# Performance work log

Hardware: AMD Instinct MI355X
Metric: run time of the kernel (lower is better)

The kernel has to match this reference:

```python
import jax, jax.numpy as jnp
import numpy as np

B, L, D = 2048, 128, 100  # utterances, max words, input_dim
H = D // 2                # LSTM hidden per direction
K = 3                     # causes per emotion in label3


def setup_inputs() -> dict:
    key = jax.random.key(0)
    ks = jax.random.split(key, 16)
    s = 1.0 / np.sqrt(H)
    inp = {
        "word_encode": jax.random.normal(ks[0], (B, L, D), jnp.float32),
        "sen_lengths": jax.random.randint(ks[1], (B, 1), 1, L + 1),
        # deterministic alternating masks -> static n_emo = n_cau = B//2
        "bi_label_emo": (jnp.arange(B) % 2 == 0).astype(jnp.int32),
        "bi_label_cau": (jnp.arange(B) % 2 == 1).astype(jnp.int32),
        "label3": jax.random.randint(ks[2], (B // 2, 1, K), 0, B // 2),
        "W_ih_f": jax.random.uniform(ks[3], (4 * H, D), jnp.float32, -s, s),
        "W_hh_f": jax.random.uniform(ks[4], (4 * H, H), jnp.float32, -s, s),
        "b_ih_f": jax.random.uniform(ks[5], (4 * H,), jnp.float32, -s, s),
        "b_hh_f": jax.random.uniform(ks[6], (4 * H,), jnp.float32, -s, s),
        "W_ih_b": jax.random.uniform(ks[7], (4 * H, D), jnp.float32, -s, s),
        "W_hh_b": jax.random.uniform(ks[8], (4 * H, H), jnp.float32, -s, s),
        "b_ih_b": jax.random.uniform(ks[9], (4 * H,), jnp.float32, -s, s),
        "b_hh_b": jax.random.uniform(ks[10], (4 * H,), jnp.float32, -s, s),
        "W3_w": jax.random.normal(ks[11], (D, 3 * D + 1), jnp.float32) * 0.05,
        "W3_b": jnp.zeros((D,), jnp.float32),
        "cls_w": jax.random.normal(ks[12], (2, D), jnp.float32) * 0.05,
        "cls_b": jnp.zeros((2,), jnp.float32),
    }
    return inp


def _lstm_cell(x, h, c, W_ih, W_hh, b_ih, b_hh):
    # PyTorch gate order: i, f, g, o
    g = x @ W_ih.T + b_ih + h @ W_hh.T + b_hh
    i, f, gg, o = jnp.split(g, 4, axis=-1)
    c_new = jax.nn.sigmoid(f) * c + jax.nn.sigmoid(i) * jnp.tanh(gg)
    h_new = jax.nn.sigmoid(o) * jnp.tanh(c_new)
    return h_new, c_new


def reference(word_encode, sen_lengths, bi_label_emo, bi_label_cau, label3,
              W_ih_f, W_hh_f, b_ih_f, b_hh_f,
              W_ih_b, W_hh_b, b_ih_b, b_hh_b,
              W3_w, W3_b, cls_w, cls_b):
    lengths = sen_lengths.reshape(-1)  # [B]
    x = word_encode.astype(jnp.float32)

    # Forward-direction LSTM over packed sequence: carry freezes past each
    # sequence's length, so the final carry h equals h at t = len-1.
    xs = jnp.swapaxes(x, 0, 1)                         # [L, B, D]
    tmask = (jnp.arange(L)[:, None] < lengths[None, :])  # [L, B]

    def step(carry, inp):
        h, c = carry
        x_t, m = inp
        h_new, c_new = _lstm_cell(x_t, h, c, W_ih_f, W_hh_f, b_ih_f, b_hh_f)
        m = m[:, None]
        return (jnp.where(m, h_new, h), jnp.where(m, c_new, c)), None

    h0 = jnp.zeros((x.shape[0], H), jnp.float32)
    (h_fwd, _), _ = jax.lax.scan(step, (h0, h0), (xs, tmask))

    # Backward direction of a packed bi-LSTM: at t = len-1 the backward cell
    # has processed exactly one token (x[len-1]) starting from zero state.
    x_last = x[jnp.arange(x.shape[0]), lengths - 1]    # [B, D]
    h_bwd, _ = _lstm_cell(x_last, h0, h0, W_ih_b, W_hh_b, b_ih_b, b_hh_b)

    U = jnp.concatenate([h_fwd, h_bwd], axis=-1)       # [B, D]

    # masks are static constants -> host-side index extraction
    emo_idx = np.flatnonzero(np.asarray(bi_label_emo))
    cau_idx = np.flatnonzero(np.asarray(bi_label_cau))
    E = U[emo_idx]                                     # [ne, D]
    C = U[cau_idx]                                     # [nc, D]
    ne, nc = E.shape[0], C.shape[0]

    # fused pairwise item_att: cat(x, y, ||x-y||_2, x*y) -> [ne, nc, 3D+1]
    Eb = jnp.broadcast_to(E[:, None, :], (ne, nc, D))
    Cb = jnp.broadcast_to(C[None, :, :], (ne, nc, D))
    diff = E[:, None, :] - C[None, :, :]
    item2 = jnp.sqrt(jnp.sum(diff * diff, axis=-1, keepdims=True))
    pair = jnp.concatenate([Eb, Cb, item2, Eb * Cb], axis=-1)
    pair = pair.reshape(ne * nc, 3 * D + 1)

    h = jax.nn.sigmoid(pair @ W3_w.T + W3_b)           # dropout = identity (eval)
    logits = h @ cls_w.T + cls_b
    p = jax.nn.log_softmax(logits, axis=1).reshape(-1, 2)

    # label_pair[j*nc + i] = 1 if i in label3[j]
    lbl = label3.reshape(ne, -1)                       # [ne, K]
    label_pair = (lbl[:, :, None] == jnp.arange(nc)[None, None, :]).any(axis=1)
    label_pair = label_pair.astype(jnp.float32).reshape(-1)
    return (p, label_pair)
```

## Files before the change

kernel.cpp:

```cpp
#include <hip/hip_runtime.h>
#include <hip/hip_bf16.h>
#include <math.h>

#define B_  2048
#define L_  128
#define D_  100
#define H_  50
#define NE  1024
#define NC  1024
#define NP  (NE*NC)
#define GSTR 212

typedef __attribute__((ext_vector_type(8))) _Float16 half8v;
typedef __attribute__((ext_vector_type(4))) _Float16 half4v;
typedef __attribute__((ext_vector_type(4))) float f32x4;

__device__ __forceinline__ float sigf(float x) { return 1.f / (1.f + __expf(-x)); }
__device__ __forceinline__ float tanhfast(float x) {
  float e = __expf(-2.f * x);
  return (1.f - e) / (1.f + e);
}
__device__ __forceinline__ void bar_sync() {
  asm volatile("s_waitcnt lgkmcnt(0)" ::: "memory");
  __builtin_amdgcn_s_barrier();
  __builtin_amdgcn_sched_barrier(0);
}

__global__ __launch_bounds__(256) void k_build_idx(const int* __restrict__ emo,
                                                   const int* __restrict__ cau,
                                                   int* __restrict__ emo_idx,
                                                   int* __restrict__ cau_idx) {
  __shared__ int pe[256], pc[256];
  int tid = threadIdx.x;
  int ce = 0, cc = 0;
  int base = tid * 8;
  for (int r = 0; r < 8; r++) { ce += (emo[base + r] != 0); cc += (cau[base + r] != 0); }
  pe[tid] = ce; pc[tid] = cc;
  __syncthreads();
  if (tid == 0) {
    int re = 0, rc = 0;
    for (int i = 0; i < 256; i++) {
      int t = pe[i]; pe[i] = re; re += t;
      t = pc[i]; pc[i] = rc; rc += t;
    }
  }
  __syncthreads();
  int oe = pe[tid], oc = pc[tid];
  for (int r = 0; r < 8; r++) {
    int idx = base + r;
    if (emo[idx] != 0) emo_idx[oe++] = idx;
    if (cau[idx] != 0) cau_idx[oc++] = idx;
  }
}

__global__ __launch_bounds__(256) void k_lstm_fwd(const float* __restrict__ x,
                                                  const int* __restrict__ lens,
                                                  const float* __restrict__ Wih,
                                                  const float* __restrict__ Whh,
                                                  const float* __restrict__ bih,
                                                  const float* __restrict__ bhh,
                                                  float* __restrict__ U) {
  __shared__ __align__(16) _Float16 Wihf[13 * 4 * 64 * 8];
  __shared__ __align__(16) _Float16 Whhf[13 * 2 * 64 * 8];
  __shared__ __align__(16) _Float16 xs[2][16 * 128];
  __shared__ __align__(16) _Float16 hs[16 * 64];
  __shared__ float gbuf[8 * GSTR];
  __shared__ float bias_l[200];
  __shared__ int len_l[8];
  int tid = threadIdx.x;
  int b0 = blockIdx.x * 8;

  for (int id = tid; id < 13 * 4 * 64; id += 256) {
    int l = id & 63, ks = (id >> 6) & 3, n = id >> 8;
    int j = n * 16 + (l & 15);
    int kb = ks * 32 + (l >> 4) * 8;
    half8v v;
    #pragma unroll
    for (int e = 0; e < 8; e++) {
      int k = kb + e;
      v[e] = (_Float16)((j < 200 && k < 100) ? Wih[j * 100 + k] : 0.f);
    }
    *(half8v*)&Wihf[id * 8] = v;
  }
  for (int id = tid; id < 13 * 2 * 64; id += 256) {
    int l = id & 63, ks = (id >> 6) & 1, n = id >> 7;
    int j = n * 16 + (l & 15);
    int kb = ks * 32 + (l >> 4) * 8;
    half8v v;
    #pragma unroll
    for (int e = 0; e < 8; e++) {
      int k = kb + e;
      v[e] = (_Float16)((j < 200 && k < 50) ? Whh[j * 50 + k] : 0.f);
    }
    *(half8v*)&Whhf[id * 8] = v;
  }
  if (tid < 200) bias_l[tid] = bih[tid] + bhh[tid];
  if (tid < 8) len_l[tid] = lens[b0 + tid];
  for (int id = tid; id < 512; id += 256) ((float4*)xs)[id] = make_float4(0.f, 0.f, 0.f, 0.f);
  for (int id = tid; id < 128; id += 256) ((float4*)hs)[id] = make_float4(0.f, 0.f, 0.f, 0.f);
  __syncthreads();

  int maxlen = 1;
  #pragma unroll
  for (int b = 0; b < 8; b++) maxlen = max(maxlen, len_l[b]);

  int wv = tid >> 6, l = tid & 63;
  int lrow = l & 15, lk = l >> 4;
  bool pvalid = tid < 200;
  int prow = tid / 25, pkq = tid % 25;

  if (pvalid) {
    float4 xv = *(const float4*)(x + (size_t)(b0 + prow) * (L_ * D_) + pkq * 4);
    half4v h4 = { (_Float16)xv.x, (_Float16)xv.y, (_Float16)xv.z, (_Float16)xv.w };
    *(half4v*)((char*)&xs[0][0] + prow * 256 + (((pkq >> 1) ^ (prow & 7)) << 4) + (pkq & 1) * 8) = h4;
  }
  __syncthreads();

  float cst[2] = {0.f, 0.f};
  for (int t = 0; t < maxlen; t++) {
    int cur = t & 1, nxt = cur ^ 1;
    float4 pf;
    if (pvalid) {
      int tp = min(t + 1, L_ - 1);
      pf = *(const float4*)(x + (size_t)(b0 + prow) * (L_ * D_) + tp * D_ + pkq * 4);
    }
    half8v ax[4], ah[2];
    #pragma unroll
    for (int ks = 0; ks < 4; ks++)
      ax[ks] = *(const half8v*)((const char*)&xs[cur][0] + lrow * 256 + (((ks * 4 + lk) ^ (lrow & 7)) << 4));
    #pragma unroll
    for (int ks = 0; ks < 2; ks++)
      ah[ks] = *(const half8v*)((const char*)hs + lrow * 128 + (((ks * 4 + lk) ^ (lrow & 7)) << 4));
    f32x4 acc[4];
    #pragma unroll
    for (int i = 0; i < 4; i++) acc[i] = (f32x4){0.f, 0.f, 0.f, 0.f};
    #pragma unroll
    for (int i = 0; i < 4; i++) {
      int n = wv + 4 * i;
      if (n < 13) {
        #pragma unroll
        for (int ks = 0; ks < 4; ks++) {
          half8v bf = *(const half8v*)&Wihf[(((n * 4 + ks) * 64) + l) * 8];
          acc[i] = __builtin_amdgcn_mfma_f32_16x16x32_f16(ax[ks], bf, acc[i], 0, 0, 0);
        }
        #pragma unroll
        for (int ks = 0; ks < 2; ks++) {
          half8v bf = *(const half8v*)&Whhf[(((n * 2 + ks) * 64) + l) * 8];
          acc[i] = __builtin_amdgcn_mfma_f32_16x16x32_f16(ah[ks], bf, acc[i], 0, 0, 0);
        }
      }
    }
    if (lk < 2) {
      #pragma unroll
      for (int i = 0; i < 4; i++) {
        int n = wv + 4 * i;
        if (n < 13) {
          #pragma unroll
          for (int q = 0; q < 4; q++)
            gbuf[(lk * 4 + q) * GSTR + n * 16 + lrow] = acc[i][q];
        }
      }
    }
    bar_sync();
    #pragma unroll
    for (int r = 0; r < 2; r++) {
      int p = tid + 256 * r;
      if (p < 400) {
        int u = p % 50, b = p / 50;
        if (t < len_l[b]) {
          float gi = gbuf[b * GSTR + u]       + bias_l[u];
          float gf = gbuf[b * GSTR + 50 + u]  + bias_l[50 + u];
          float gg = gbuf[b * GSTR + 100 + u] + bias_l[100 + u];
          float go = gbuf[b * GSTR + 150 + u] + bias_l[150 + u];
          float cn = sigf(gf) * cst[r] + sigf(gi) * tanhfast(gg);
          cst[r] = cn;
          float hv = sigf(go) * tanhfast(cn);
          *(_Float16*)((char*)hs + b * 128 + (((u >> 3) ^ (b & 7)) << 4) + (u & 7) * 2) = (_Float16)hv;
          if (t == len_l[b] - 1) U[(size_t)(b0 + b) * 100 + u] = hv;
        }
      }
    }
    if (pvalid) {
      half4v h4 = { (_Float16)pf.x, (_Float16)pf.y, (_Float16)pf.z, (_Float16)pf.w };
      *(half4v*)((char*)&xs[nxt][0] + prow * 256 + (((pkq >> 1) ^ (prow & 7)) << 4) + (pkq & 1) * 8) = h4;
    }
    bar_sync();
  }
}

__global__ __launch_bounds__(256) void k_lstm_bwd(const float* __restrict__ x,
                                                  const int* __restrict__ lens,
                                                  const float* __restrict__ Wih,
                                                  const float* __restrict__ bih,
                                                  const float* __restrict__ bhh,
                                                  float* __restrict__ U) {
  __shared__ float W_l[100][200];
  __shared__ float bias_l[200];
  __shared__ float xs[8][100];
  __shared__ float gb[8][200];
  __shared__ int len_l[8];
  int tid = threadIdx.x;
  int b0 = blockIdx.x * 8;
  for (int id = tid; id < 20000; id += 256) { int j = id / 100, i = id % 100; W_l[i][j] = Wih[id]; }
  if (tid < 200) bias_l[tid] = bih[tid] + bhh[tid];
  if (tid < 8) len_l[tid] = lens[b0 + tid];
  __syncthreads();
  for (int id = tid; id < 800; id += 256) {
    int b = id / 100, i = id % 100;
    int t = len_l[b] - 1;
    xs[b][i] = x[(size_t)(b0 + b) * (L_ * D_) + t * D_ + i];
  }
  __syncthreads();
  int j = tid;
  if (j < 200) {
    float acc[8];
    float bj = bias_l[j];
    #pragma unroll
    for (int b = 0; b < 8; b++) acc[b] = bj;
    #pragma unroll 2
    for (int k = 0; k < 100; k++) {
      float w = W_l[k][j];
      #pragma unroll
      for (int b = 0; b < 8; b++) acc[b] = fmaf(w, xs[b][k], acc[b]);
    }
    #pragma unroll
    for (int b = 0; b < 8; b++) gb[b][j] = acc[b];
  }
  __syncthreads();
  if (tid < 200) {
    int uk = tid % 50, ub = tid / 50;
    #pragma unroll
    for (int s = 0; s < 2; s++) {
      int b = ub + 4 * s;
      float gi = gb[b][uk], gg = gb[b][100 + uk], go = gb[b][150 + uk];
      float cn = sigf(gi) * tanhfast(gg);
      U[(size_t)(b0 + b) * 100 + 50 + uk] = sigf(go) * tanhfast(cn);
    }
  }
}

__global__ __launch_bounds__(128) void k_prep(const float* __restrict__ U,
                                              const int* __restrict__ emo_idx,
                                              const int* __restrict__ cau_idx,
                                              const float* __restrict__ W3w,
                                              float* __restrict__ A,
                                              float* __restrict__ En,
                                              float* __restrict__ Cn,
                                              _Float16* __restrict__ Cfrag) {
  __shared__ float u[100];
  int bid = blockIdx.x;
  int tid = threadIdx.x;
  bool is_e = bid < NE;
  int i = is_e ? bid : bid - NE;
  int row = is_e ? emo_idx[i] : cau_idx[i];
  if (tid < 100) u[tid] = U[row * 100 + tid];
  __syncthreads();
  if (is_e && tid < 100) {
    float acc = 0.f;
    const float* wrow = W3w + tid * 301;
    #pragma unroll 4
    for (int k = 0; k < 100; k++) acc = fmaf(u[k], wrow[k], acc);
    A[i * 100 + tid] = acc;
  }
  if (!is_e && tid < 16) {
    int ct = i >> 4, lrow = i & 15;
    int ks = tid >> 2, seg = tid & 3;
    half8v v;
    #pragma unroll
    for (int e2 = 0; e2 < 8; e2++) {
      int k = tid * 8 + e2;
      v[e2] = (_Float16)((k < 100) ? u[k] : 0.f);
    }
    *(half8v*)(Cfrag + ((size_t)((ct * 4 + ks) * 64 + lrow + 16 * seg)) * 8) = v;
  }
  if (tid < 64) {
    float v = u[tid] * u[tid];
    if (tid < 36) v += u[tid + 64] * u[tid + 64];
    for (int o = 32; o > 0; o >>= 1) v += __shfl_down(v, o);
    if (tid == 0) { if (is_e) En[i] = v; else Cn[i] = v; }
  }
}

__global__ __launch_bounds__(256) void k_pair(const float* __restrict__ U,
                                              const int* __restrict__ emo_idx,
                                              const float* __restrict__ A,
                                              const float* __restrict__ En,
                                              const float* __restrict__ Cn,
                                              const float* __restrict__ W3w,
                                              const float* __restrict__ W3b,
                                              const float* __restrict__ clsw,
                                              const float* __restrict__ clsb,
                                              const int* __restrict__ label3,
                                              const _Float16* __restrict__ Cfrag,
                                              float* __restrict__ out) {
  __shared__ __align__(16) _Float16 Bbf[7 * 4 * 64 * 8];
  __shared__ float E_l[100];
  __shared__ float addA[112], wd_l[112];
  __shared__ float Cn_l[1024];
  __shared__ float clsw_l[200];
  __shared__ float clsb_l[2];
  __shared__ int   lbl_l[3];
  __shared__ float En_s;

  int tid = threadIdx.x;
  int e = blockIdx.x;
  int erow = emo_idx[e];

  if (tid < 100) E_l[tid] = U[erow * 100 + tid];
  if (tid < 112) {
    bool v = tid < 100;
    addA[tid] = v ? (A[e * 100 + tid] + W3b[tid]) : 0.f;
    wd_l[tid] = v ? W3w[tid * 301 + 200] : 0.f;
  }
  for (int id = tid; id < 1024; id += 256) Cn_l[id] = Cn[id];
  if (tid < 200) clsw_l[tid] = clsw[tid];
  if (tid < 2) clsb_l[tid] = clsb[tid];
  if (tid < 3) lbl_l[tid] = label3[e * 3 + tid];
  if (tid == 0) En_s = En[e];
  __syncthreads();

  for (int id = tid; id < 1792; id += 256) {
    int l = id & 63, ks = (id >> 6) & 3, dt = id >> 8;
    int d = dt * 16 + (l & 15);
    int kb = ks * 32 + (l >> 4) * 8;
    half8v v;
    #pragma unroll
    for (int m = 0; m < 8; m++) {
      int k = kb + m;
      float f = 0.f;
      if (k < 100) {
        if (d < 100)       f = W3w[d * 301 + 201 + k] * E_l[k] + W3w[d * 301 + 100 + k];
        else if (d == 100) f = E_l[k];
      }
      v[m] = (_Float16)f;
    }
    *(half8v*)&Bbf[id * 8] = v;
  }
  __syncthreads();

  int wv = tid >> 6, l = tid & 63;
  int lrow = l & 15, lk = l >> 4;
  for (int g = 0; g < 4; g++) {
    int ctb = wv * 16 + g * 4;
    f32x4 acc[4][7];
    #pragma unroll
    for (int tt = 0; tt < 4; tt++)
      #pragma unroll
      for (int dt = 0; dt < 7; dt++) acc[tt][dt] = (f32x4){0.f, 0.f, 0.f, 0.f};
    #pragma unroll
    for (int ks = 0; ks < 4; ks++) {
      half8v af[4];
      #pragma unroll
      for (int tt = 0; tt < 4; tt++)
        af[tt] = *(const half8v*)(Cfrag + ((size_t)(((ctb + tt) * 4 + ks) * 64 + l)) * 8);
      #pragma unroll
      for (int dt = 0; dt < 7; dt++) {
        half8v bf = *(const half8v*)&Bbf[((dt * 4 + ks) * 64 + l) * 8];
        #pragma unroll
        for (int tt = 0; tt < 4; tt++)
          acc[tt][dt] = __builtin_amdgcn_mfma_f32_16x16x32_f16(af[tt], bf, acc[tt][dt], 0, 0, 0);
      }
    }
    #pragma unroll
    for (int tt = 0; tt < 4; tt++) {
      int ct = ctb + tt;
      float dist[4];
      #pragma unroll
      for (int r = 0; r < 4; r++) {
        float dotv = __shfl(acc[tt][6][r], (l & 48) + 4, 64);
        int c = ct * 16 + lk * 4 + r;
        float d2 = En_s + Cn_l[c] - 2.f * dotv;
        dist[r] = sqrtf(fmaxf(d2, 0.f));
      }
      float l0[4] = {0.f, 0.f, 0.f, 0.f}, l1[4] = {0.f, 0.f, 0.f, 0.f};
      #pragma unroll
      for (int dt = 0; dt < 7; dt++) {
        int d = dt * 16 + lrow;
        float av = addA[d], wdv = wd_l[d];
        bool valid = d < 100;
        float cw0 = valid ? clsw_l[d] : 0.f;
        float cw1 = valid ? clsw_l[100 + d] : 0.f;
        #pragma unroll
        for (int r = 0; r < 4; r++) {
          float z = acc[tt][dt][r] + av + dist[r] * wdv;
          float h = sigf(z);
          l0[r] = fmaf(h, cw0, l0[r]);
          l1[r] = fmaf(h, cw1, l1[r]);
        }
      }
      #pragma unroll
      for (int off = 1; off < 16; off <<= 1) {
        #pragma unroll
        for (int r = 0; r < 4; r++) {
          l0[r] += __shfl_xor(l0[r], off, 64);
          l1[r] += __shfl_xor(l1[r], off, 64);
        }
      }
      if (lrow == 0) {
        #pragma unroll
        for (int r = 0; r < 4; r++) {
          int c = ct * 16 + lk * 4 + r;
          float a0 = l0[r] + clsb_l[0], a1 = l1[r] + clsb_l[1];
          float mx = fmaxf(a0, a1);
          float lse = mx + __logf(__expf(a0 - mx) + __expf(a1 - mx));
          int pair = e * 1024 + c;
          out[pair * 2]     = a0 - lse;
          out[pair * 2 + 1] = a1 - lse;
          out[2 * NP + pair] = (lbl_l[0] == c || lbl_l[1] == c || lbl_l[2] == c) ? 1.f : 0.f;
        }
      }
    }
  }
}

extern "C" void kernel_launch(void* const* d_in, const int* in_sizes, int n_in,
                              void* d_out, int out_size, void* d_ws, size_t ws_size,
                              hipStream_t stream) {
  const float* x     = (const float*)d_in[0];
  const int*   lens  = (const int*)d_in[1];
  const int*   emo   = (const int*)d_in[2];
  const int*   cau   = (const int*)d_in[3];
  const int*   lbl3  = (const int*)d_in[4];
  const float* Wih_f = (const float*)d_in[5];
  const float* Whh_f = (const float*)d_in[6];
  const float* bih_f = (const float*)d_in[7];
  const float* bhh_f = (const float*)d_in[8];
  const float* Wih_b = (const float*)d_in[9];
  const float* bih_b = (const float*)d_in[11];
  const float* bhh_b = (const float*)d_in[12];
  const float* W3w   = (const float*)d_in[13];
  const float* W3b   = (const float*)d_in[14];
  const float* clsw  = (const float*)d_in[15];
  const float* clsb  = (const float*)d_in[16];
  float* out = (float*)d_out;

  char* ws = (char*)d_ws;
  float*     U       = (float*)ws;
  int*       emo_idx = (int*)(ws + 819200);
  int*       cau_idx = (int*)(ws + 823296);
  float*     A       = (float*)(ws + 827392);
  float*     En      = (float*)(ws + 1236992);
  float*     Cn      = (float*)(ws + 1241088);
  _Float16*  Cfrag   = (_Float16*)(ws + 1245184);

  hipLaunchKernelGGL(k_build_idx, dim3(1), dim3(256), 0, stream, emo, cau, emo_idx, cau_idx);
  hipLaunchKernelGGL(k_lstm_fwd, dim3(256), dim3(256), 0, stream,
                     x, lens, Wih_f, Whh_f, bih_f, bhh_f, U);
  hipLaunchKernelGGL(k_lstm_bwd, dim3(256), dim3(256), 0, stream,
                     x, lens, Wih_b, bih_b, bhh_b, U);
  hipLaunchKernelGGL(k_prep, dim3(2048), dim3(128), 0, stream,
                     U, emo_idx, cau_idx, W3w, A, En, Cn, Cfrag);
  hipLaunchKernelGGL(k_pair, dim3(1024), dim3(256), 0, stream,
                     U, emo_idx, A, En, Cn, W3w, W3b, clsw, clsb, lbl3, Cfrag, out);
}
```

Before: 635.9 us.

## Precompute weight fragments once, widen LSTM block, shrink pair tiling, scan-based index build

Adds a k_wfrag kernel that converts the LSTM and W3 weights into MFMA fragment layouts once, so LSTM and pair blocks copy them instead of rebuilding them per block. The forward LSTM moves to 1024-thread blocks with one wave per gate tile and one thread per hidden unit, which is meant to shorten the serial per-step critical path. k_pair now builds its B operand with vectorized FMAs from the precomputed buffers, uses 2 instead of 4 C tiles per iteration to cut register pressure, and declares a 4-block occupancy target. k_build_idx replaces its serial prefix sum with a wave-shuffle scan, and k_prep reads a transposed W1. WfG reuses A's workspace region, which is only safe because k_lstm_fwd finishes before k_prep writes A.

```diff
diff --git a/kernel.cpp b/kernel.cpp
--- a/kernel.cpp
+++ b/kernel.cpp
@@ -26,42 +26,98 @@
   __builtin_amdgcn_sched_barrier(0);
 }
 
+__global__ __launch_bounds__(256) void k_wfrag(const float* __restrict__ Wih,
+                                               const float* __restrict__ Whh,
+                                               const float* __restrict__ W3w,
+                                               _Float16* __restrict__ WfG,
+                                               float* __restrict__ W4f,
+                                               float* __restrict__ W2f,
+                                               float* __restrict__ W1T,
+                                               float* __restrict__ Wd) {
+  int gid = blockIdx.x * 256 + threadIdx.x;
+  int nthr = gridDim.x * 256;
+  for (int id = gid; id < 4992; id += nthr) {
+    half8v v;
+    if (id < 3328) {
+      int l = id & 63, ks = (id >> 6) & 3, n = id >> 8;
+      int j = n * 16 + (l & 15), kb = ks * 32 + (l >> 4) * 8;
+      #pragma unroll
+      for (int e = 0; e < 8; e++) {
+        int k = kb + e;
+        v[e] = (_Float16)((j < 200 && k < 100) ? Wih[j * 100 + k] : 0.f);
+      }
+    } else {
+      int id2 = id - 3328;
+      int l = id2 & 63, ks = (id2 >> 6) & 1, n = id2 >> 7;
+      int j = n * 16 + (l & 15), kb = ks * 32 + (l >> 4) * 8;
+      #pragma unroll
+      for (int e = 0; e < 8; e++) {
+        int k = kb + e;
+        v[e] = (_Float16)((j < 200 && k < 50) ? Whh[j * 50 + k] : 0.f);
+      }
+    }
+    *(half8v*)(WfG + (size_t)id * 8) = v;
+  }
+  for (int id = gid; id < 1792; id += nthr) {
+    int l = id & 63, ks = (id >> 6) & 3, dt = id >> 8;
+    int d = dt * 16 + (l & 15), kb = ks * 32 + (l >> 4) * 8;
+    #pragma unroll
+    for (int m = 0; m < 8; m++) {
+      int k = kb + m;
+      float w4 = 0.f, w2 = 0.f;
+      if (k < 100) {
+        if (d < 100)       { w4 = W3w[d * 301 + 201 + k]; w2 = W3w[d * 301 + 100 + k]; }
+        else if (d == 100) { w4 = 1.f; }
+      }
+      W4f[(size_t)id * 8 + m] = w4;
+      W2f[(size_t)id * 8 + m] = w2;
+    }
+  }
+  for (int id = gid; id < 10000; id += nthr) {
+    int k = id / 100, d = id % 100;
+    W1T[id] = W3w[d * 301 + k];
+  }
+  for (int id = gid; id < 100; id += nthr) Wd[id] = W3w[id * 301 + 200];
+}
+
 __global__ __launch_bounds__(256) void k_build_idx(const int* __restrict__ emo,
                                                    const int* __restrict__ cau,
                                                    int* __restrict__ emo_idx,
                                                    int* __restrict__ cau_idx) {
-  __shared__ int pe[256], pc[256];
-  int tid = threadIdx.x;
+  __shared__ int wsum_e[4], wsum_c[4];
+  int tid = threadIdx.x, lane = tid & 63, wv = tid >> 6;
+  int base = tid * 8;
+  int fe[8], fc[8];
   int ce = 0, cc = 0;
-  int base = tid * 8;
-  for (int r = 0; r < 8; r++) { ce += (emo[base + r] != 0); cc += (cau[base + r] != 0); }
-  pe[tid] = ce; pc[tid] = cc;
-  __syncthreads();
-  if (tid == 0) {
-    int re = 0, rc = 0;
-    for (int i = 0; i < 256; i++) {
-      int t = pe[i]; pe[i] = re; re += t;
-      t = pc[i]; pc[i] = rc; rc += t;
-    }
-  }
-  __syncthreads();
-  int oe = pe[tid], oc = pc[tid];
+  #pragma unroll
   for (int r = 0; r < 8; r++) {
-    int idx = base + r;
-    if (emo[idx] != 0) emo_idx[oe++] = idx;
-    if (cau[idx] != 0) cau_idx[oc++] = idx;
-  }
-}
-
-__global__ __launch_bounds__(256) void k_lstm_fwd(const float* __restrict__ x,
-                                                  const int* __restrict__ lens,
-                                                  const float* __restrict__ Wih,
-                                                  const float* __restrict__ Whh,
-                                                  const float* __restrict__ bih,
-                                                  const float* __restrict__ bhh,
-                                                  float* __restrict__ U) {
-  __shared__ __align__(16) _Float16 Wihf[13 * 4 * 64 * 8];
-  __shared__ __align__(16) _Float16 Whhf[13 * 2 * 64 * 8];
+    fe[r] = (emo[base + r] != 0); ce += fe[r];
+    fc[r] = (cau[base + r] != 0); cc += fc[r];
+  }
+  int se = ce, sc = cc;
+  for (int o = 1; o < 64; o <<= 1) {
+    int ve = __shfl_up(se, o), vc = __shfl_up(sc, o);
+    if (lane >= o) { se += ve; sc += vc; }
+  }
+  if (lane == 63) { wsum_e[wv] = se; wsum_c[wv] = sc; }
+  __syncthreads();
+  int obe = 0, obc = 0;
+  for (int w = 0; w < wv; w++) { obe += wsum_e[w]; obc += wsum_c[w]; }
+  int oe = obe + se - ce, oc = obc + sc - cc;
+  #pragma unroll
+  for (int r = 0; r < 8; r++) {
+    if (fe[r]) emo_idx[oe++] = base + r;
+    if (fc[r]) cau_idx[oc++] = base + r;
+  }
+}
+
+__global__ __launch_bounds__(1024) void k_lstm_fwd(const float* __restrict__ x,
+                                                   const int* __restrict__ lens,
+                                                   const _Float16* __restrict__ WfG,
+                                                   const float* __restrict__ bih,
+                                                   const float* __restrict__ bhh,
+                                                   float* __restrict__ U) {
+  __shared__ __align__(16) _Float16 Wf[4992 * 8];
   __shared__ __align__(16) _Float16 xs[2][16 * 128];
   __shared__ __align__(16) _Float16 hs[16 * 64];
   __shared__ float gbuf[8 * GSTR];
@@ -70,34 +126,12 @@
   int tid = threadIdx.x;
   int b0 = blockIdx.x * 8;
 
-  for (int id = tid; id < 13 * 4 * 64; id += 256) {
-    int l = id & 63, ks = (id >> 6) & 3, n = id >> 8;
-    int j = n * 16 + (l & 15);
-    int kb = ks * 32 + (l >> 4) * 8;
-    half8v v;
-    #pragma unroll
-    for (int e = 0; e < 8; e++) {
-      int k = kb + e;
-      v[e] = (_Float16)((j < 200 && k < 100) ? Wih[j * 100 + k] : 0.f);
-    }
-    *(half8v*)&Wihf[id * 8] = v;
-  }
-  for (int id = tid; id < 13 * 2 * 64; id += 256) {
-    int l = id & 63, ks = (id >> 6) & 1, n = id >> 7;
-    int j = n * 16 + (l & 15);
-    int kb = ks * 32 + (l >> 4) * 8;
-    half8v v;
-    #pragma unroll
-    for (int e = 0; e < 8; e++) {
-      int k = kb + e;
-      v[e] = (_Float16)((j < 200 && k < 50) ? Whh[j * 50 + k] : 0.f);
-    }
-    *(half8v*)&Whhf[id * 8] = v;
-  }
+  for (int id = tid; id < 4992; id += 1024)
+    ((float4*)Wf)[id] = ((const float4*)WfG)[id];
   if (tid < 200) bias_l[tid] = bih[tid] + bhh[tid];
   if (tid < 8) len_l[tid] = lens[b0 + tid];
-  for (int id = tid; id < 512; id += 256) ((float4*)xs)[id] = make_float4(0.f, 0.f, 0.f, 0.f);
-  for (int id = tid; id < 128; id += 256) ((float4*)hs)[id] = make_float4(0.f, 0.f, 0.f, 0.f);
+  for (int id = tid; id < 512; id += 1024) ((float4*)xs)[id] = make_float4(0.f, 0.f, 0.f, 0.f);
+  for (int id = tid; id < 128; id += 1024) ((float4*)hs)[id] = make_float4(0.f, 0.f, 0.f, 0.f);
   __syncthreads();
 
   int maxlen = 1;
@@ -106,8 +140,10 @@
 
   int wv = tid >> 6, l = tid & 63;
   int lrow = l & 15, lk = l >> 4;
-  bool pvalid = tid < 200;
-  int prow = tid / 25, pkq = tid % 25;
+  bool pvalid = tid >= 824;
+  int pidx = pvalid ? (tid - 824) : 0;
+  int prow = pidx / 25, pkq = pidx % 25;
+  int u_ = tid % 50, b_ = tid / 50;
 
   if (pvalid) {
     float4 xv = *(const float4*)(x + (size_t)(b0 + prow) * (L_ * D_) + pkq * 4);
@@ -116,7 +152,7 @@
   }
   __syncthreads();
 
-  float cst[2] = {0.f, 0.f};
+  float cstate = 0.f;
   for (int t = 0; t < maxlen; t++) {
     int cur = t & 1, nxt = cur ^ 1;
     float4 pf;
@@ -124,61 +160,42 @@
       int tp = min(t + 1, L_ - 1);
       pf = *(const float4*)(x + (size_t)(b0 + prow) * (L_ * D_) + tp * D_ + pkq * 4);
     }
-    half8v ax[4], ah[2];
-    #pragma unroll
-    for (int ks = 0; ks < 4; ks++)
-      ax[ks] = *(const half8v*)((const char*)&xs[cur][0] + lrow * 256 + (((ks * 4 + lk) ^ (lrow & 7)) << 4));
-    #pragma unroll
-    for (int ks = 0; ks < 2; ks++)
-      ah[ks] = *(const half8v*)((const char*)hs + lrow * 128 + (((ks * 4 + lk) ^ (lrow & 7)) << 4));
-    f32x4 acc[4];
-    #pragma unroll
-    for (int i = 0; i < 4; i++) acc[i] = (f32x4){0.f, 0.f, 0.f, 0.f};
-    #pragma unroll
-    for (int i = 0; i < 4; i++) {
-      int n = wv + 4 * i;
-      if (n < 13) {
+    if (wv < 13) {
+      half8v ax[4], ah[2];
+      #pragma unroll
+      for (int ks = 0; ks < 4; ks++)
+        ax[ks] = *(const half8v*)((const char*)&xs[cur][0] + lrow * 256 + (((ks * 4 + lk) ^ (lrow & 7)) << 4));
+      #pragma unroll
+      for (int ks = 0; ks < 2; ks++)
+        ah[ks] = *(const half8v*)((const char*)hs + lrow * 128 + (((ks * 4 + lk) ^ (lrow & 7)) << 4));
+      f32x4 acc = (f32x4){0.f, 0.f, 0.f, 0.f};
+      #pragma unroll
+      for (int ks = 0; ks < 4; ks++) {
+        half8v bf = *(const half8v*)&Wf[(size_t)((wv * 4 + ks) * 64 + l) * 8];
+        acc = __builtin_amdgcn_mfma_f32_16x16x32_f16(ax[ks], bf, acc, 0, 0, 0);
+      }
+      #pragma unroll
+      for (int ks = 0; ks < 2; ks++) {
+        half8v bf = *(const half8v*)&Wf[(size_t)(3328 + (wv * 2 + ks) * 64 + l) * 8];
+        acc = __builtin_amdgcn_mfma_f32_16x16x32_f16(ah[ks], bf, acc, 0, 0, 0);
+      }
+      if (lk < 2) {
         #pragma unroll
-        for (int ks = 0; ks < 4; ks++) {
-          half8v bf = *(const half8v*)&Wihf[(((n * 4 + ks) * 64) + l) * 8];
-          acc[i] = __builtin_amdgcn_mfma_f32_16x16x32_f16(ax[ks], bf, acc[i], 0, 0, 0);
-        }
-        #pragma unroll
-        for (int ks = 0; ks < 2; ks++) {
-          half8v bf = *(const half8v*)&Whhf[(((n * 2 + ks) * 64) + l) * 8];
-          acc[i] = __builtin_amdgcn_mfma_f32_16x16x32_f16(ah[ks], bf, acc[i], 0, 0, 0);
-        }
-      }
-    }
-    if (lk < 2) {
-      #pragma unroll
-      for (int i = 0; i < 4; i++) {
-        int n = wv + 4 * i;
-        if (n < 13) {
-          #pragma unroll
-          for (int q = 0; q < 4; q++)
-            gbuf[(lk * 4 + q) * GSTR + n * 16 + lrow] = acc[i][q];
-        }
+        for (int q = 0; q < 4; q++)
+          gbuf[(lk * 4 + q) * GSTR + wv * 16 + lrow] = acc[q];
       }
     }
     bar_sync();
-    #pragma unroll
-    for (int r = 0; r < 2; r++) {
-      int p = tid + 256 * r;
-      if (p < 400) {
-        int u = p % 50, b = p / 50;
-        if (t < len_l[b]) {
-          float gi = gbuf[b * GSTR + u]       + bias_l[u];
-          float gf = gbuf[b * GSTR + 50 + u]  + bias_l[50 + u];
-          float gg = gbuf[b * GSTR + 100 + u] + bias_l[100 + u];
-          float go = gbuf[b * GSTR + 150 + u] + bias_l[150 + u];
-          float cn = sigf(gf) * cst[r] + sigf(gi) * tanhfast(gg);
-          cst[r] = cn;
-          float hv = sigf(go) * tanhfast(cn);
-          *(_Float16*)((char*)hs + b * 128 + (((u >> 3) ^ (b & 7)) << 4) + (u & 7) * 2) = (_Float16)hv;
-          if (t == len_l[b] - 1) U[(size_t)(b0 + b) * 100 + u] = hv;
-        }
-      }
+    if (tid < 400 && t < len_l[b_]) {
+      float gi = gbuf[b_ * GSTR + u_]       + bias_l[u_];
+      float gf = gbuf[b_ * GSTR + 50 + u_]  + bias_l[50 + u_];
+      float gg = gbuf[b_ * GSTR + 100 + u_] + bias_l[100 + u_];
+      float go = gbuf[b_ * GSTR + 150 + u_] + bias_l[150 + u_];
+      float cn = sigf(gf) * cstate + sigf(gi) * tanhfast(gg);
+      cstate = cn;
+      float hv = sigf(go) * tanhfast(cn);
+      *(_Float16*)((char*)hs + b_ * 128 + (((u_ >> 3) ^ (b_ & 7)) << 4) + (u_ & 7) * 2) = (_Float16)hv;
+      if (t == len_l[b_] - 1) U[(size_t)(b0 + b_) * 100 + u_] = hv;
     }
     if (pvalid) {
       half4v h4 = { (_Float16)pf.x, (_Float16)pf.y, (_Float16)pf.z, (_Float16)pf.w };
@@ -242,7 +259,7 @@
 __global__ __launch_bounds__(128) void k_prep(const float* __restrict__ U,
                                               const int* __restrict__ emo_idx,
                                               const int* __restrict__ cau_idx,
-                                              const float* __restrict__ W3w,
+                                              const float* __restrict__ W1T,
                                               float* __restrict__ A,
                                               float* __restrict__ En,
                                               float* __restrict__ Cn,
@@ -257,9 +274,8 @@
   __syncthreads();
   if (is_e && tid < 100) {
     float acc = 0.f;
-    const float* wrow = W3w + tid * 301;
     #pragma unroll 4
-    for (int k = 0; k < 100; k++) acc = fmaf(u[k], wrow[k], acc);
+    for (int k = 0; k < 100; k++) acc = fmaf(u[k], W1T[k * 100 + tid], acc);
     A[i * 100 + tid] = acc;
   }
   if (!is_e && tid < 16) {
@@ -281,20 +297,22 @@
   }
 }
 
-__global__ __launch_bounds__(256) void k_pair(const float* __restrict__ U,
-                                              const int* __restrict__ emo_idx,
-                                              const float* __restrict__ A,
-                                              const float* __restrict__ En,
-                                              const float* __restrict__ Cn,
-                                              const float* __restrict__ W3w,
-                                              const float* __restrict__ W3b,
-                                              const float* __restrict__ clsw,
-                                              const float* __restrict__ clsb,
-                                              const int* __restrict__ label3,
-                                              const _Float16* __restrict__ Cfrag,
-                                              float* __restrict__ out) {
-  __shared__ __align__(16) _Float16 Bbf[7 * 4 * 64 * 8];
-  __shared__ float E_l[100];
+__global__ __launch_bounds__(256, 4) void k_pair(const float* __restrict__ U,
+                                                 const int* __restrict__ emo_idx,
+                                                 const float* __restrict__ A,
+                                                 const float* __restrict__ En,
+                                                 const float* __restrict__ Cn,
+                                                 const float* __restrict__ W4f,
+                                                 const float* __restrict__ W2f,
+                                                 const float* __restrict__ Wd,
+                                                 const float* __restrict__ W3b,
+                                                 const float* __restrict__ clsw,
+                                                 const float* __restrict__ clsb,
+                                                 const int* __restrict__ label3,
+                                                 const _Float16* __restrict__ Cfrag,
+                                                 float* __restrict__ out) {
+  __shared__ __align__(16) _Float16 Bbf[1792 * 8];
+  __shared__ __align__(16) float E_l[128];
   __shared__ float addA[112], wd_l[112];
   __shared__ float Cn_l[1024];
   __shared__ float clsw_l[200];
@@ -306,63 +324,63 @@
   int e = blockIdx.x;
   int erow = emo_idx[e];
 
-  if (tid < 100) E_l[tid] = U[erow * 100 + tid];
+  if (tid < 128) E_l[tid] = (tid < 100) ? U[erow * 100 + tid] : 0.f;
   if (tid < 112) {
     bool v = tid < 100;
     addA[tid] = v ? (A[e * 100 + tid] + W3b[tid]) : 0.f;
-    wd_l[tid] = v ? W3w[tid * 301 + 200] : 0.f;
-  }
-  for (int id = tid; id < 1024; id += 256) Cn_l[id] = Cn[id];
+    wd_l[tid] = v ? Wd[tid] : 0.f;
+  }
   if (tid < 200) clsw_l[tid] = clsw[tid];
   if (tid < 2) clsb_l[tid] = clsb[tid];
   if (tid < 3) lbl_l[tid] = label3[e * 3 + tid];
   if (tid == 0) En_s = En[e];
+  {
+    float4 cv = ((const float4*)Cn)[tid];
+    *(float4*)&Cn_l[tid * 4] = cv;
+  }
   __syncthreads();
 
   for (int id = tid; id < 1792; id += 256) {
-    int l = id & 63, ks = (id >> 6) & 3, dt = id >> 8;
-    int d = dt * 16 + (l & 15);
-    int kb = ks * 32 + (l >> 4) * 8;
-    half8v v;
-    #pragma unroll
-    for (int m = 0; m < 8; m++) {
-      int k = kb + m;
-      float f = 0.f;
-      if (k < 100) {
-        if (d < 100)       f = W3w[d * 301 + 201 + k] * E_l[k] + W3w[d * 301 + 100 + k];
-        else if (d == 100) f = E_l[k];
-      }
-      v[m] = (_Float16)f;
-    }
-    *(half8v*)&Bbf[id * 8] = v;
+    int l = id & 63;
+    int kb = ((id >> 6) & 3) * 32 + (l >> 4) * 8;
+    float4 wa = ((const float4*)W4f)[id * 2], wb = ((const float4*)W4f)[id * 2 + 1];
+    float4 va = ((const float4*)W2f)[id * 2], vb = ((const float4*)W2f)[id * 2 + 1];
+    float4 ea = *(const float4*)&E_l[kb],     eb = *(const float4*)&E_l[kb + 4];
+    half8v h;
+    h[0] = (_Float16)fmaf(wa.x, ea.x, va.x);
+    h[1] = (_Float16)fmaf(wa.y, ea.y, va.y);
+    h[2] = (_Float16)fmaf(wa.z, ea.z, va.z);
+    h[3] = (_Float16)fmaf(wa.w, ea.w, va.w);
+    h[4] = (_Float16)fmaf(wb.x, eb.x, vb.x);
+    h[5] = (_Float16)fmaf(wb.y, eb.y, vb.y);
+    h[6] = (_Float16)fmaf(wb.z, eb.z, vb.z);
+    h[7] = (_Float16)fmaf(wb.w, eb.w, vb.w);
+    *(half8v*)&Bbf[(size_t)id * 8] = h;
   }
   __syncthreads();
 
   int wv = tid >> 6, l = tid & 63;
   int lrow = l & 15, lk = l >> 4;
-  for (int g = 0; g < 4; g++) {
-    int ctb = wv * 16 + g * 4;
-    f32x4 acc[4][7];
-    #pragma unroll
-    for (int tt = 0; tt < 4; tt++)
+  for (int g = 0; g < 8; g++) {
+    int ctb = wv * 16 + g * 2;
+    f32x4 acc[2][7];
+    #pragma unroll
+    for (int tt = 0; tt < 2; tt++)
       #pragma unroll
       for (int dt = 0; dt < 7; dt++) acc[tt][dt] = (f32x4){0.f, 0.f, 0.f, 0.f};
     #pragma unroll
     for (int ks = 0; ks < 4; ks++) {
-      half8v af[4];
-      #pragma unroll
-      for (int tt = 0; tt < 4; tt++)
-        af[tt] = *(const half8v*)(Cfrag + ((size_t)(((ctb + tt) * 4 + ks) * 64 + l)) * 8);
+      half8v af0 = *(const half8v*)(Cfrag + ((size_t)((ctb * 4 + ks) * 64 + l)) * 8);
+      half8v af1 = *(const half8v*)(Cfrag + ((size_t)(((ctb + 1) * 4 + ks) * 64 + l)) * 8);
       #pragma unroll
       for (int dt = 0; dt < 7; dt++) {
-        half8v bf = *(const half8v*)&Bbf[((dt * 4 + ks) * 64 + l) * 8];
-        #pragma unroll
-        for (int tt = 0; tt < 4; tt++)
-          acc[tt][dt] = __builtin_amdgcn_mfma_f32_16x16x32_f16(af[tt], bf, acc[tt][dt], 0, 0, 0);
-      }
-    }
-    #pragma unroll
-    for (int tt = 0; tt < 4; tt++) {
+        half8v bf = *(const half8v*)&Bbf[(size_t)((dt * 4 + ks) * 64 + l) * 8];
+        acc[0][dt] = __builtin_amdgcn_mfma_f32_16x16x32_f16(af0, bf, acc[0][dt], 0, 0, 0);
+        acc[1][dt] = __builtin_amdgcn_mfma_f32_16x16x32_f16(af1, bf, acc[1][dt], 0, 0, 0);
+      }
+    }
+    #pragma unroll
+    for (int tt = 0; tt < 2; tt++) {
       int ct = ctb + tt;
       float dist[4];
       #pragma unroll
@@ -439,17 +457,24 @@
   int*       emo_idx = (int*)(ws + 819200);
   int*       cau_idx = (int*)(ws + 823296);
   float*     A       = (float*)(ws + 827392);
+  _Float16*  WfG     = (_Float16*)(ws + 827392);
   float*     En      = (float*)(ws + 1236992);
   float*     Cn      = (float*)(ws + 1241088);
   _Float16*  Cfrag   = (_Float16*)(ws + 1245184);
-
+  float*     W4f     = (float*)(ws + 1507328);
+  float*     W2f     = (float*)(ws + 1564672);
+  float*     W1T     = (float*)(ws + 1622016);
+  float*     Wd      = (float*)(ws + 1662016);
+
+  hipLaunchKernelGGL(k_wfrag, dim3(64), dim3(256), 0, stream,
+                     Wih_f, Whh_f, W3w, WfG, W4f, W2f, W1T, Wd);
   hipLaunchKernelGGL(k_build_idx, dim3(1), dim3(256), 0, stream, emo, cau, emo_idx, cau_idx);
-  hipLaunchKernelGGL(k_lstm_fwd, dim3(256), dim3(256), 0, stream,
-                     x, lens, Wih_f, Whh_f, bih_f, bhh_f, U);
+  hipLaunchKernelGGL(k_lstm_fwd, dim3(256), dim3(1024), 0, stream,
+                     x, lens, WfG, bih_f, bhh_f, U);
   hipLaunchKernelGGL(k_lstm_bwd, dim3(256), dim3(256), 0, stream,
                      x, lens, Wih_b, bih_b, bhh_b, U);
   hipLaunchKernelGGL(k_prep, dim3(2048), dim3(128), 0, stream,
-                     U, emo_idx, cau_idx, W3w, A, En, Cn, Cfrag);
+                     U, emo_idx, cau_idx, W1T, A, En, Cn, Cfrag);
   hipLaunchKernelGGL(k_pair, dim3(1024), dim3(256), 0, stream,
-                     U, emo_idx, A, En, Cn, W3w, W3b, clsw, clsb, lbl3, Cfrag, out);
-}
+                     U, emo_idx, A, En, Cn, W4f, W2f, Wd, W3b, clsw, clsb, lbl3, Cfrag, out);
+}
```

After: 581.8 us. 8.5% less time.
